# Performance work log

Hardware: AMD Instinct MI355X
Metric: run time of the kernel (lower is better)

## Reference

```python
import jax, jax.numpy as jnp
import numpy as np

N_NODES = 1_000_000
NUM_GRAPHS = 512
IN_DIM = 128
ASSIGN_DIM = 128
N_EDGES = 2_000_000


def setup_inputs() -> dict:
    key = jax.random.key(0)
    kx, ke, kw1, kb1, kw2, kb2 = jax.random.split(key, 6)
    x = jax.random.normal(kx, (N_NODES, IN_DIM), dtype=jnp.float32)
    edge_index = jax.random.randint(ke, (2, N_EDGES), 0, N_NODES, dtype=jnp.int64)
    # sorted, contiguous graph ids covering all NUM_GRAPHS segments (equal sizes)
    batch = (jnp.arange(N_NODES, dtype=jnp.int64) * NUM_GRAPHS) // N_NODES
    W1 = jax.random.normal(kw1, (IN_DIM, ASSIGN_DIM), dtype=jnp.float32) * 0.02
    b1 = jax.random.normal(kb1, (ASSIGN_DIM,), dtype=jnp.float32) * 0.02
    W2 = jax.random.normal(kw2, (ASSIGN_DIM, ASSIGN_DIM), dtype=jnp.float32) * 0.02
    b2 = jax.random.normal(kb2, (ASSIGN_DIM,), dtype=jnp.float32) * 0.02
    return {"x": x, "edge_index": edge_index, "batch": batch,
            "W1": W1, "b1": b1, "W2": W2, "b2": b2}


def reference(x, edge_index, batch, W1, b1, W2, b2):
    # assign_matrix: Linear(input_dim -> assign_dim)
    assign_score = x @ W1 + b1                      # [N, assign_dim]
    h = assign_score @ W2 + b2                      # [N, assign_dim]
    # per-graph mean pooling: single-pass segment sum / counts
    sums = jax.ops.segment_sum(h, batch, num_segments=NUM_GRAPHS)   # [B, assign_dim]
    counts = jax.ops.segment_sum(jnp.ones((h.shape[0],), dtype=h.dtype),
                                 batch, num_segments=NUM_GRAPHS)    # [B]
    pooled_x = sums / counts[:, None]
    return (pooled_x, edge_index, batch)
```

## Files before the change

kernel.cpp:

```cpp
#include <hip/hip_runtime.h>

#define DIM 128
#define NUM_GRAPHS 512

typedef float f4 __attribute__((ext_vector_type(4)));

__device__ __forceinline__ void flush_acc(float* __restrict__ sums,
                                          float* __restrict__ counts,
                                          int g, int chunk, f4 a, float run) {
    float* s = sums + (size_t)g * DIM + chunk * 4;
    atomicAdd(s + 0, a[0]); atomicAdd(s + 1, a[1]);
    atomicAdd(s + 2, a[2]); atomicAdd(s + 3, a[3]);
    if (chunk == 0) atomicAdd(counts + g, run);
}

__global__ __launch_bounds__(256) void seg_sum_kernel(
    const float* __restrict__ x, const int* __restrict__ batch,
    float* __restrict__ sums, float* __restrict__ counts, int n_nodes)
{
    const int NPT = 64;
    int chunk = threadIdx.x & 31;
    int group = threadIdx.x >> 5;
    long long node0 = (long long)blockIdx.x * 512 + (long long)group * NPT;
    if (node0 >= n_nodes) return;
    int cnt = NPT;
    if (node0 + NPT > n_nodes) cnt = (int)(n_nodes - node0);

    const f4* __restrict__ xv = (const f4*)x;
    const f4* __restrict__ p = xv + node0 * 32 + chunk;

    int g0 = batch[node0];
    int g1 = batch[node0 + cnt - 1];

    if (g0 == g1) {
        f4 a = (f4)0.f, b = (f4)0.f;
        int i = 0;
        #pragma unroll 4
        for (; i + 1 < cnt; i += 2) {
            f4 v0 = __builtin_nontemporal_load(p + (long long)i * 32);
            f4 v1 = __builtin_nontemporal_load(p + (long long)(i + 1) * 32);
            a += v0; b += v1;
        }
        if (i < cnt) a += __builtin_nontemporal_load(p + (long long)i * 32);
        flush_acc(sums, counts, g0, chunk, a + b, (float)cnt);
    } else if (g1 - g0 == 1) {
        int lo = 1, hi = cnt - 1;
        while (lo < hi) {
            int mid = (lo + hi) >> 1;
            if (batch[node0 + mid] == g0) lo = mid + 1; else hi = mid;
        }
        f4 a = (f4)0.f;
        for (int i = 0; i < lo; ++i)
            a += __builtin_nontemporal_load(p + (long long)i * 32);
        flush_acc(sums, counts, g0, chunk, a, (float)lo);
        a = (f4)0.f;
        for (int i = lo; i < cnt; ++i)
            a += __builtin_nontemporal_load(p + (long long)i * 32);
        flush_acc(sums, counts, g1, chunk, a, (float)(cnt - lo));
    } else {
        f4 a = (f4)0.f;
        int cur = g0; float run = 0.f;
        for (int i = 0; i < cnt; ++i) {
            int g = batch[node0 + i];
            if (g != cur) {
                flush_acc(sums, counts, cur, chunk, a, run);
                cur = g; a = (f4)0.f; run = 0.f;
            }
            a += __builtin_nontemporal_load(p + (long long)i * 32);
            run += 1.f;
        }
        flush_acc(sums, counts, cur, chunk, a, run);
    }
}

__global__ __launch_bounds__(DIM) void mlp_kernel(
    const float* __restrict__ sums, const float* __restrict__ counts,
    const float* __restrict__ W1, const float* __restrict__ b1,
    const float* __restrict__ W2, const float* __restrict__ b2,
    float* __restrict__ out)
{
    __shared__ float xrow[DIM];
    __shared__ float yrow[DIM];
    int g = blockIdx.x;
    int t = threadIdx.x;
    float inv_cnt = 1.0f / counts[g];
    xrow[t] = sums[(size_t)g * DIM + t] * inv_cnt;
    __syncthreads();
    float acc = b1[t];
    #pragma unroll 8
    for (int k = 0; k < DIM; ++k) acc += xrow[k] * W1[k * DIM + t];
    yrow[t] = acc;
    __syncthreads();
    float acc2 = b2[t];
    #pragma unroll 8
    for (int k = 0; k < DIM; ++k) acc2 += yrow[k] * W2[k * DIM + t];
    out[(size_t)g * DIM + t] = acc2;
}

__global__ __launch_bounds__(256) void copy2_i2f(
    const int4* __restrict__ e, float4* __restrict__ eo, long long ne4,
    const int4* __restrict__ b, float4* __restrict__ bo, long long nb4)
{
    long long i = (long long)blockIdx.x * blockDim.x + threadIdx.x;
    if (i < ne4) {
        int4 v = e[i];
        eo[i] = make_float4((float)v.x, (float)v.y, (float)v.z, (float)v.w);
    } else {
        long long j = i - ne4;
        if (j < nb4) {
            int4 v = b[j];
            bo[j] = make_float4((float)v.x, (float)v.y, (float)v.z, (float)v.w);
        }
    }
}

extern "C" void kernel_launch(void* const* d_in, const int* in_sizes, int n_in,
                              void* d_out, int out_size, void* d_ws, size_t ws_size,
                              hipStream_t stream) {
    const float* x     = (const float*)d_in[0];
    const int*   edge  = (const int*)d_in[1];
    const int*   batch = (const int*)d_in[2];
    const float* W1    = (const float*)d_in[3];
    const float* b1    = (const float*)d_in[4];
    const float* W2    = (const float*)d_in[5];
    const float* b2    = (const float*)d_in[6];
    float* out = (float*)d_out;

    long long edge_n  = in_sizes[1];
    long long n_nodes = in_sizes[2];

    float* sums   = (float*)d_ws;
    float* counts = sums + (size_t)NUM_GRAPHS * DIM;

    hipMemsetAsync(d_ws, 0, ((size_t)NUM_GRAPHS * DIM + NUM_GRAPHS) * sizeof(float), stream);

    int blocksA = (int)((n_nodes + 511) / 512);
    seg_sum_kernel<<<blocksA, 256, 0, stream>>>(x, batch, sums, counts, (int)n_nodes);

    mlp_kernel<<<NUM_GRAPHS, DIM, 0, stream>>>(sums, counts, W1, b1, W2, b2, out);

    float* edge_out  = out + (size_t)NUM_GRAPHS * DIM;
    float* batch_out = edge_out + edge_n;
    long long ne4 = edge_n >> 2, nb4 = n_nodes >> 2;
    int blocksC = (int)((ne4 + nb4 + 255) / 256);
    copy2_i2f<<<blocksC, 256, 0, stream>>>((const int4*)edge, (float4*)edge_out, ne4,
                                           (const int4*)batch, (float4*)batch_out, nb4);
}
```

Baseline: 704.7 us.

## Replace atomic segment sums with per-block partials and fuse copy into stage one

Each 512-node block now reduces its nodes in shared memory into at most two partial sums, for its first and last graph ids, and writes them to workspace. A second kernel finds each graph's blocks by binary search, combines the partials and applies the MLP. This removes the memset and the global float atomics. The int-to-float copy of edges and batch now runs as extra blocks of the first kernel with nontemporal stores, saving a launch. Blocks that span more than two graphs are handled by rescanning x inside stage two, which could be slow if segments were small.

New measurement: 705.6 us. No clear change (+0.1%).

```diff
diff --git a/kernel.cpp b/kernel.cpp
--- a/kernel.cpp
+++ b/kernel.cpp
@@ -2,89 +2,167 @@
 
 #define DIM 128
 #define NUM_GRAPHS 512
+#define NPB 512
+#define NPT 64
 
 typedef float f4 __attribute__((ext_vector_type(4)));
-
-__device__ __forceinline__ void flush_acc(float* __restrict__ sums,
-                                          float* __restrict__ counts,
-                                          int g, int chunk, f4 a, float run) {
-    float* s = sums + (size_t)g * DIM + chunk * 4;
-    atomicAdd(s + 0, a[0]); atomicAdd(s + 1, a[1]);
-    atomicAdd(s + 2, a[2]); atomicAdd(s + 3, a[3]);
-    if (chunk == 0) atomicAdd(counts + g, run);
-}
-
-__global__ __launch_bounds__(256) void seg_sum_kernel(
+typedef int   i4 __attribute__((ext_vector_type(4)));
+
+__device__ __forceinline__ void route(f4 s, float n, int gg, int bg0, int bg1,
+                                      f4& acc0, f4& acc1, float& c0, float& c1) {
+    if (gg == bg0)      { acc0 += s; c0 += n; }
+    else if (gg == bg1) { acc1 += s; c1 += n; }
+}
+
+__global__ __launch_bounds__(256) void stage1_kernel(
     const float* __restrict__ x, const int* __restrict__ batch,
-    float* __restrict__ sums, float* __restrict__ counts, int n_nodes)
+    int2* __restrict__ gids, float2* __restrict__ cnts,
+    float* __restrict__ p0, float* __restrict__ p1,
+    int n_nodes, int nb,
+    const i4* __restrict__ e, f4* __restrict__ eo, long long ne4,
+    const i4* __restrict__ bt, f4* __restrict__ bo, long long nb4)
 {
-    const int NPT = 64;
-    int chunk = threadIdx.x & 31;
-    int group = threadIdx.x >> 5;
-    long long node0 = (long long)blockIdx.x * 512 + (long long)group * NPT;
-    if (node0 >= n_nodes) return;
-    int cnt = NPT;
-    if (node0 + NPT > n_nodes) cnt = (int)(n_nodes - node0);
-
-    const f4* __restrict__ xv = (const f4*)x;
-    const f4* __restrict__ p = xv + node0 * 32 + chunk;
-
-    int g0 = batch[node0];
-    int g1 = batch[node0 + cnt - 1];
-
-    if (g0 == g1) {
-        f4 a = (f4)0.f, b = (f4)0.f;
-        int i = 0;
-        #pragma unroll 4
-        for (; i + 1 < cnt; i += 2) {
-            f4 v0 = __builtin_nontemporal_load(p + (long long)i * 32);
-            f4 v1 = __builtin_nontemporal_load(p + (long long)(i + 1) * 32);
-            a += v0; b += v1;
-        }
-        if (i < cnt) a += __builtin_nontemporal_load(p + (long long)i * 32);
-        flush_acc(sums, counts, g0, chunk, a + b, (float)cnt);
-    } else if (g1 - g0 == 1) {
-        int lo = 1, hi = cnt - 1;
-        while (lo < hi) {
-            int mid = (lo + hi) >> 1;
-            if (batch[node0 + mid] == g0) lo = mid + 1; else hi = mid;
-        }
-        f4 a = (f4)0.f;
-        for (int i = 0; i < lo; ++i)
-            a += __builtin_nontemporal_load(p + (long long)i * 32);
-        flush_acc(sums, counts, g0, chunk, a, (float)lo);
-        a = (f4)0.f;
-        for (int i = lo; i < cnt; ++i)
-            a += __builtin_nontemporal_load(p + (long long)i * 32);
-        flush_acc(sums, counts, g1, chunk, a, (float)(cnt - lo));
-    } else {
-        f4 a = (f4)0.f;
-        int cur = g0; float run = 0.f;
-        for (int i = 0; i < cnt; ++i) {
-            int g = batch[node0 + i];
-            if (g != cur) {
-                flush_acc(sums, counts, cur, chunk, a, run);
-                cur = g; a = (f4)0.f; run = 0.f;
-            }
-            a += __builtin_nontemporal_load(p + (long long)i * 32);
-            run += 1.f;
-        }
-        flush_acc(sums, counts, cur, chunk, a, run);
-    }
-}
-
-__global__ __launch_bounds__(DIM) void mlp_kernel(
-    const float* __restrict__ sums, const float* __restrict__ counts,
+    __shared__ float s0[8][DIM];
+    __shared__ float s1[8][DIM];
+    __shared__ float sc[8][2];
+
+    if ((int)blockIdx.x >= nb) {
+        long long i = (long long)(blockIdx.x - nb) * 256 + threadIdx.x;
+        if (i < ne4) {
+            i4 v = __builtin_nontemporal_load(e + i);
+            f4 o = { (float)v.x, (float)v.y, (float)v.z, (float)v.w };
+            __builtin_nontemporal_store(o, eo + i);
+        } else {
+            long long j = i - ne4;
+            if (j < nb4) {
+                i4 v = __builtin_nontemporal_load(bt + j);
+                f4 o = { (float)v.x, (float)v.y, (float)v.z, (float)v.w };
+                __builtin_nontemporal_store(o, bo + j);
+            }
+        }
+        return;
+    }
+
+    const int chunk = threadIdx.x & 31;
+    const int group = threadIdx.x >> 5;
+    const int blk   = blockIdx.x;
+    const long long base  = (long long)blk * NPB;
+    const long long node0 = base + (long long)group * NPT;
+    long long blast = base + NPB; if (blast > n_nodes) blast = n_nodes;
+    const int bg0 = batch[base];
+    const int bg1 = batch[blast - 1];
+
+    f4 acc0 = (f4)0.f, acc1 = (f4)0.f;
+    float c0 = 0.f, c1 = 0.f;
+
+    if (node0 < n_nodes) {
+        int cnt = NPT;
+        if (node0 + NPT > n_nodes) cnt = (int)(n_nodes - node0);
+        const f4* __restrict__ p = (const f4*)x + node0 * 32 + chunk;
+
+        int g0 = batch[node0];
+        int g1 = batch[node0 + cnt - 1];
+
+        if (g0 == g1) {
+            f4 a = (f4)0.f, b = (f4)0.f;
+            int i = 0;
+            #pragma unroll 4
+            for (; i + 1 < cnt; i += 2) {
+                f4 v0 = __builtin_nontemporal_load(p + (long long)i * 32);
+                f4 v1 = __builtin_nontemporal_load(p + (long long)(i + 1) * 32);
+                a += v0; b += v1;
+            }
+            if (i < cnt) a += __builtin_nontemporal_load(p + (long long)i * 32);
+            route(a + b, (float)cnt, g0, bg0, bg1, acc0, acc1, c0, c1);
+        } else if (g1 - g0 == 1) {
+            int lo = 1, hi = cnt - 1;
+            while (lo < hi) {
+                int mid = (lo + hi) >> 1;
+                if (batch[node0 + mid] == g0) lo = mid + 1; else hi = mid;
+            }
+            f4 a = (f4)0.f;
+            for (int i = 0; i < lo; ++i)
+                a += __builtin_nontemporal_load(p + (long long)i * 32);
+            route(a, (float)lo, g0, bg0, bg1, acc0, acc1, c0, c1);
+            a = (f4)0.f;
+            for (int i = lo; i < cnt; ++i)
+                a += __builtin_nontemporal_load(p + (long long)i * 32);
+            route(a, (float)(cnt - lo), g1, bg0, bg1, acc0, acc1, c0, c1);
+        } else {
+            for (int i = 0; i < cnt; ++i) {
+                int g = batch[node0 + i];
+                f4 v = __builtin_nontemporal_load(p + (long long)i * 32);
+                route(v, 1.f, g, bg0, bg1, acc0, acc1, c0, c1);
+            }
+        }
+    }
+
+    *(f4*)&s0[group][chunk * 4] = acc0;
+    *(f4*)&s1[group][chunk * 4] = acc1;
+    if (chunk == 0) { sc[group][0] = c0; sc[group][1] = c1; }
+    __syncthreads();
+
+    #pragma unroll
+    for (int st = 4; st >= 1; st >>= 1) {
+        if (group < st) {
+            *(f4*)&s0[group][chunk * 4] += *(const f4*)&s0[group + st][chunk * 4];
+            *(f4*)&s1[group][chunk * 4] += *(const f4*)&s1[group + st][chunk * 4];
+            if (chunk < 2) sc[group][chunk] += sc[group + st][chunk];
+        }
+        __syncthreads();
+    }
+
+    if (group == 0) {
+        *(f4*)(p0 + (size_t)blk * DIM + chunk * 4) = *(const f4*)&s0[0][chunk * 4];
+    } else if (group == 1) {
+        *(f4*)(p1 + (size_t)blk * DIM + chunk * 4) = *(const f4*)&s1[0][chunk * 4];
+    } else if (group == 2 && chunk == 0) {
+        gids[blk] = make_int2(bg0, bg1);
+        cnts[blk] = make_float2(sc[0][0], sc[0][1]);
+    }
+}
+
+__global__ __launch_bounds__(DIM) void stage2_kernel(
+    const int2* __restrict__ gids, const float2* __restrict__ cnts,
+    const float* __restrict__ p0, const float* __restrict__ p1,
+    const float* __restrict__ x, const int* __restrict__ batch,
+    int n_nodes, int nb,
     const float* __restrict__ W1, const float* __restrict__ b1,
     const float* __restrict__ W2, const float* __restrict__ b2,
     float* __restrict__ out)
 {
     __shared__ float xrow[DIM];
     __shared__ float yrow[DIM];
-    int g = blockIdx.x;
-    int t = threadIdx.x;
-    float inv_cnt = 1.0f / counts[g];
-    xrow[t] = sums[(size_t)g * DIM + t] * inv_cnt;
+    const int g = blockIdx.x;
+    const int t = threadIdx.x;
+
+    int lo, hi;
+    { int a = 0, b = nb - 1;
+      while (a < b) { int m = (a + b) >> 1; if (gids[m].y < g) a = m + 1; else b = m; }
+      lo = a; }
+    { int a = 0, b = nb - 1;
+      while (a < b) { int m = (a + b + 1) >> 1; if (gids[m].x > g) b = m - 1; else a = m; }
+      hi = a; }
+
+    float sum = 0.f, cnt = 0.f;
+    for (int b = lo; b <= hi; ++b) {
+        const int2 id = gids[b];
+        const float2 c = cnts[b];
+        if (id.x == g) { sum += p0[(size_t)b * DIM + t]; cnt += c.x; }
+        if (id.y == g && id.y != id.x) { sum += p1[(size_t)b * DIM + t]; cnt += c.y; }
+        if (id.x < g && g < id.y) {
+            long long s = (long long)b * NPB;
+            long long e2 = s + NPB; if (e2 > n_nodes) e2 = n_nodes;
+            long long a1 = s, bb = e2;
+            while (a1 < bb) { long long m = (a1 + bb) >> 1; if (batch[m] <  g) a1 = m + 1; else bb = m; }
+            long long a2 = a1, bb2 = e2;
+            while (a2 < bb2) { long long m = (a2 + bb2) >> 1; if (batch[m] <= g) a2 = m + 1; else bb2 = m; }
+            for (long long nidx = a1; nidx < a2; ++nidx) sum += x[nidx * DIM + t];
+            cnt += (float)(a2 - a1);
+        }
+    }
+
+    xrow[t] = sum / cnt;
     __syncthreads();
     float acc = b1[t];
     #pragma unroll 8
@@ -95,23 +173,6 @@
     #pragma unroll 8
     for (int k = 0; k < DIM; ++k) acc2 += yrow[k] * W2[k * DIM + t];
     out[(size_t)g * DIM + t] = acc2;
-}
-
-__global__ __launch_bounds__(256) void copy2_i2f(
-    const int4* __restrict__ e, float4* __restrict__ eo, long long ne4,
-    const int4* __restrict__ b, float4* __restrict__ bo, long long nb4)
-{
-    long long i = (long long)blockIdx.x * blockDim.x + threadIdx.x;
-    if (i < ne4) {
-        int4 v = e[i];
-        eo[i] = make_float4((float)v.x, (float)v.y, (float)v.z, (float)v.w);
-    } else {
-        long long j = i - ne4;
-        if (j < nb4) {
-            int4 v = b[j];
-            bo[j] = make_float4((float)v.x, (float)v.y, (float)v.z, (float)v.w);
-        }
-    }
 }
 
 extern "C" void kernel_launch(void* const* d_in, const int* in_sizes, int n_in,
@@ -128,21 +189,25 @@
 
     long long edge_n  = in_sizes[1];
     long long n_nodes = in_sizes[2];
-
-    float* sums   = (float*)d_ws;
-    float* counts = sums + (size_t)NUM_GRAPHS * DIM;
-
-    hipMemsetAsync(d_ws, 0, ((size_t)NUM_GRAPHS * DIM + NUM_GRAPHS) * sizeof(float), stream);
-
-    int blocksA = (int)((n_nodes + 511) / 512);
-    seg_sum_kernel<<<blocksA, 256, 0, stream>>>(x, batch, sums, counts, (int)n_nodes);
-
-    mlp_kernel<<<NUM_GRAPHS, DIM, 0, stream>>>(sums, counts, W1, b1, W2, b2, out);
+    int nb = (int)((n_nodes + NPB - 1) / NPB);
+
+    char* w = (char*)d_ws;
+    int2*   gids = (int2*)w;   w += ((size_t)nb * sizeof(int2)        + 255) & ~(size_t)255;
+    float2* cnts = (float2*)w; w += ((size_t)nb * sizeof(float2)      + 255) & ~(size_t)255;
+    float*  p0   = (float*)w;  w += ((size_t)nb * DIM * sizeof(float) + 255) & ~(size_t)255;
+    float*  p1   = (float*)w;
 
     float* edge_out  = out + (size_t)NUM_GRAPHS * DIM;
     float* batch_out = edge_out + edge_n;
     long long ne4 = edge_n >> 2, nb4 = n_nodes >> 2;
-    int blocksC = (int)((ne4 + nb4 + 255) / 256);
-    copy2_i2f<<<blocksC, 256, 0, stream>>>((const int4*)edge, (float4*)edge_out, ne4,
-                                           (const int4*)batch, (float4*)batch_out, nb4);
-}
+    int ncopy = (int)((ne4 + nb4 + 255) / 256);
+
+    stage1_kernel<<<nb + ncopy, 256, 0, stream>>>(
+        x, batch, gids, cnts, p0, p1, (int)n_nodes, nb,
+        (const i4*)edge, (f4*)edge_out, ne4,
+        (const i4*)batch, (f4*)batch_out, nb4);
+
+    stage2_kernel<<<NUM_GRAPHS, DIM, 0, stream>>>(
+        gids, cnts, p0, p1, x, batch, (int)n_nodes, nb,
+        W1, b1, W2, b2, out);
+}
```
